# Optimization experiments

Measured on AMD Instinct MI355X. Metric: run time of the kernel, lower is better.

## Reference

```python
import jax, jax.numpy as jnp
import numpy as np

N, E, CIN, HOPS, HID, COUT = 50000, 800000, 64, 3, 256, 64

def setup_inputs() -> dict:
    key = jax.random.key(0)
    ks = jax.random.split(key, 8)
    x = jax.random.normal(ks[0], (N, CIN), dtype=jnp.float32)
    edge_index = jax.random.randint(ks[1], (2, E), 0, N, dtype=jnp.int64)
    def lin(k, fan_in, fan_out):
        bound = 1.0 / np.sqrt(fan_in)
        return jax.random.uniform(k, (fan_in, fan_out), jnp.float32, -bound, bound)
    W0 = lin(ks[2], CIN * (HOPS + 1), HID)
    W1 = lin(ks[3], HID, HID)
    W2 = lin(ks[4], HID, COUT)
    b0 = jnp.zeros((HID,), jnp.float32)
    b1 = jnp.zeros((HID,), jnp.float32)
    b2 = jnp.zeros((COUT,), jnp.float32)
    return {"x": x, "edge_index": edge_index, "W0": W0, "b0": b0, "W1": W1, "b1": b1, "W2": W2, "b2": b2}

def reference(x, edge_index, W0, b0, W1, b1, W2, b2):
    row, col = edge_index[0], edge_index[1]
    n = x.shape[0]
    # degree of destination nodes (degree(col, N))
    d = jax.ops.segment_sum(jnp.ones_like(col, dtype=jnp.float32), col, num_segments=n)
    d_norm_in = 1.0 / jnp.sqrt(d[col])   # per-edge
    d_norm_out = 1.0 / jnp.sqrt(d[row])
    value = d_norm_in * d_norm_out
    value = jnp.where(jnp.isfinite(value), value, 0.0)  # nan_to_num
    def spmm(h):
        # adj has entries at (col[e], row[e]) -> out[i] = sum_{e: col[e]=i} value[e] * h[row[e]]
        return jax.ops.segment_sum(value[:, None] * h[row], col, num_segments=n)
    emb = [x]
    h = x
    for _ in range(HOPS):
        h = spmm(h)
        emb.append(h)
    z = jnp.concatenate(emb, axis=1)  # [N, CIN*(HOPS+1)]
    # eval mode: dropout is identity, use_bn=False
    z = jax.nn.relu(z @ W0 + b0)
    z = jax.nn.relu(z @ W1 + b1)
    return z @ W2 + b2
```

## Files before the change

kernel.cpp:

```cpp
#include <hip/hip_runtime.h>


#define ZW 256
#define NCH 64

typedef __attribute__((ext_vector_type(8))) __bf16 bf16x8;
typedef __attribute__((ext_vector_type(4))) float f32x4;
typedef __attribute__((ext_vector_type(4))) unsigned short us4;

__device__ __forceinline__ unsigned f2bf(float f) {
    unsigned x = __float_as_uint(f);
    return (x + 0x7fffu + ((x >> 16) & 1u)) >> 16;
}
__device__ __forceinline__ unsigned pack_split(float v) {
    unsigned hb = f2bf(v);
    float hf = __uint_as_float(hb << 16);
    unsigned lb = f2bf(v - hf);
    return (hb << 16) | lb;
}
__device__ __forceinline__ float unpack_f(unsigned u) {
    return __uint_as_float(u & 0xffff0000u) + __uint_as_float(u << 16);
}


__global__ void init_kernel(const float* __restrict__ x, unsigned* __restrict__ zp,
                            int* __restrict__ deg, int N) {
    int stride = gridDim.x * blockDim.x;
    int total4 = N * 16;
    for (int idx = blockIdx.x * blockDim.x + threadIdx.x; idx < total4; idx += stride) {
        int n = idx >> 4, c4 = idx & 15;
        float4 v = *reinterpret_cast<const float4*>(x + (size_t)n * NCH + c4 * 4);
        uint4 o;
        o.x = pack_split(v.x); o.y = pack_split(v.y);
        o.z = pack_split(v.z); o.w = pack_split(v.w);
        *reinterpret_cast<uint4*>(zp + (size_t)n * ZW + c4 * 4) = o;
    }
    for (int idx = blockIdx.x * blockDim.x + threadIdx.x; idx < N; idx += stride)
        deg[idx] = 0;
}

__global__ void degree_kernel(const int* __restrict__ col, int* __restrict__ deg, int E) {
    int stride = gridDim.x * blockDim.x;
    for (int e = blockIdx.x * blockDim.x + threadIdx.x; e < E; e += stride)
        atomicAdd(&deg[col[e]], 1);
}

__global__ __launch_bounds__(1024) void scan_part_kernel(const int* __restrict__ deg,
                                                         int* __restrict__ off,
                                                         int* __restrict__ bsum, int N) {
    __shared__ int smem[1024];
    int tid = threadIdx.x;
    int i = blockIdx.x * 1024 + tid;
    int v = (i < N) ? deg[i] : 0;
    smem[tid] = v;
    __syncthreads();
    for (int o = 1; o < 1024; o <<= 1) {
        int t = (tid >= o) ? smem[tid - o] : 0;
        __syncthreads();
        smem[tid] += t;
        __syncthreads();
    }
    if (i < N) off[i] = smem[tid] - v;
    if (tid == 1023) bsum[blockIdx.x] = smem[1023];
}

__global__ void scan_tops_kernel(const int* __restrict__ bsum, int* __restrict__ btot, int nb) {
    int lane = threadIdx.x;
    int v = (lane < nb) ? bsum[lane] : 0;
    int incl = v;
    for (int o = 1; o < 64; o <<= 1) {
        int t = __shfl_up(incl, o);
        if (lane >= o) incl += t;
    }
    if (lane < nb) btot[lane] = incl - v;
    if (lane == 63) btot[nb] = incl;
}

__global__ __launch_bounds__(1024) void scan_add_kernel(int* __restrict__ off,
                                                        int* __restrict__ cur,
                                                        const int* __restrict__ btot,
                                                        int N, int nb) {
    int i = blockIdx.x * 1024 + threadIdx.x;
    if (i < N) {
        int o = off[i] + btot[blockIdx.x];
        off[i] = o;
        cur[i] = o;
    }
    if (i == 0) off[N] = btot[nb];
}

__global__ void scatter_kernel(const int* __restrict__ row, const int* __restrict__ col,
                               const int* __restrict__ deg, int* __restrict__ cursor,
                               int2* __restrict__ meta, int E) {
    int stride = gridDim.x * blockDim.x;
    for (int e = blockIdx.x * blockDim.x + threadIdx.x; e < E; e += stride) {
        int r = row[e];
        int c = col[e];
        int dc = deg[c];
        int dr = deg[r];
        float v = 0.0f;
        if (dc > 0 && dr > 0) v = rsqrtf((float)(dc * dr));
        int pos = atomicAdd(&cursor[c], 1);
        meta[pos] = make_int2(r, __float_as_int(v));
    }
}

__global__ void spmm_csr_kernel(const int* __restrict__ offsets, const int2* __restrict__ meta,
                                const unsigned* __restrict__ zin, unsigned* __restrict__ zout,
                                int N) {
    int lane = threadIdx.x & 63;
    int wave = (blockIdx.x * blockDim.x + threadIdx.x) >> 6;
    if (wave >= N) return;
    int start = offsets[wave];
    int end   = offsets[wave + 1];
    float acc = 0.0f;
    int j = start;
    for (; j + 2 <= end; j += 2) {
        int2 m0 = meta[j];
        int2 m1 = meta[j + 1];
        float h0 = unpack_f(zin[(size_t)m0.x * ZW + lane]);
        float h1 = unpack_f(zin[(size_t)m1.x * ZW + lane]);
        acc = fmaf(__int_as_float(m0.y), h0, acc);
        acc = fmaf(__int_as_float(m1.y), h1, acc);
    }
    if (j < end) {
        int2 m0 = meta[j];
        acc = fmaf(__int_as_float(m0.y), unpack_f(zin[(size_t)m0.x * ZW + lane]), acc);
    }
    zout[(size_t)wave * ZW + lane] = pack_split(acc);
}

__global__ void prep_w_kernel(const float* __restrict__ W0, const float* __restrict__ W1,
                              const float* __restrict__ W2, unsigned short* __restrict__ ws) {
    int idx = blockIdx.x * blockDim.x + threadIdx.x;
    if (idx >= 65536) return;
    int n = idx >> 8, k = idx & 255;
    unsigned p0 = pack_split(W0[(size_t)k * 256 + n]);
    ws[idx]          = (unsigned short)(p0 >> 16);
    ws[65536 + idx]  = (unsigned short)(p0 & 0xffff);
    unsigned p1 = pack_split(W1[(size_t)k * 256 + n]);
    ws[131072 + idx] = (unsigned short)(p1 >> 16);
    ws[196608 + idx] = (unsigned short)(p1 & 0xffff);
    if (idx < 16384) {
        int n2 = idx >> 8, k2 = idx & 255;
        unsigned p2 = pack_split(W2[(size_t)k2 * 64 + n2]);
        ws[262144 + idx] = (unsigned short)(p2 >> 16);
        ws[278528 + idx] = (unsigned short)(p2 & 0xffff);
    }
}

__global__ __launch_bounds__(256) void gemm256_kernel(
        const unsigned* __restrict__ Ap, const unsigned short* __restrict__ Wh,
        const unsigned short* __restrict__ Wl, const float* __restrict__ bias,
        unsigned* __restrict__ Cp, int M) {
    __shared__ unsigned short Ah[128][40];
    __shared__ unsigned short Al[128][40];
    __shared__ unsigned short Bh[128][40];
    __shared__ unsigned short Bl[128][40];

    int tid = threadIdx.x;
    int lane = tid & 63;
    int wid = tid >> 6;
    int wr = wid >> 1, wc = wid & 1;
    int bm = blockIdx.x * 128;
    int bn = blockIdx.y * 128;
    int l15 = lane & 15, kg = lane >> 4;

    f32x4 acc[4][4] = {};

    for (int k0 = 0; k0 < 256; k0 += 32) {
#pragma unroll
        for (int it = 0; it < 4; ++it) {
            int idx = it * 256 + tid;
            int row = idx >> 3, ch = idx & 7;
            int grow = bm + row; if (grow > M - 1) grow = M - 1;
            uint4 q = *reinterpret_cast<const uint4*>(Ap + (size_t)grow * 256 + k0 + ch * 4);
            us4 hi, lo;
            hi.x = (unsigned short)(q.x >> 16); lo.x = (unsigned short)q.x;
            hi.y = (unsigned short)(q.y >> 16); lo.y = (unsigned short)q.y;
            hi.z = (unsigned short)(q.z >> 16); lo.z = (unsigned short)q.z;
            hi.w = (unsigned short)(q.w >> 16); lo.w = (unsigned short)q.w;
            *reinterpret_cast<us4*>(&Ah[row][ch * 4]) = hi;
            *reinterpret_cast<us4*>(&Al[row][ch * 4]) = lo;
        }
#pragma unroll
        for (int it = 0; it < 2; ++it) {
            int idx = it * 256 + tid;
            int n = idx >> 2, ch = idx & 3;
            *reinterpret_cast<uint4*>(&Bh[n][ch * 8]) =
                *reinterpret_cast<const uint4*>(Wh + (size_t)(bn + n) * 256 + k0 + ch * 8);
            *reinterpret_cast<uint4*>(&Bl[n][ch * 8]) =
                *reinterpret_cast<const uint4*>(Wl + (size_t)(bn + n) * 256 + k0 + ch * 8);
        }
        __syncthreads();

        bf16x8 ah[4], al[4], bh[4], bl[4];
#pragma unroll
        for (int m = 0; m < 4; ++m) {
            int r = wr * 64 + m * 16 + l15;
            ah[m] = *reinterpret_cast<const bf16x8*>(&Ah[r][kg * 8]);
            al[m] = *reinterpret_cast<const bf16x8*>(&Al[r][kg * 8]);
        }
#pragma unroll
        for (int n = 0; n < 4; ++n) {
            int c = wc * 64 + n * 16 + l15;
            bh[n] = *reinterpret_cast<const bf16x8*>(&Bh[c][kg * 8]);
            bl[n] = *reinterpret_cast<const bf16x8*>(&Bl[c][kg * 8]);
        }
#pragma unroll
        for (int m = 0; m < 4; ++m)
#pragma unroll
            for (int n = 0; n < 4; ++n) {
                acc[m][n] = __builtin_amdgcn_mfma_f32_16x16x32_bf16(ah[m], bh[n], acc[m][n], 0, 0, 0);
                acc[m][n] = __builtin_amdgcn_mfma_f32_16x16x32_bf16(ah[m], bl[n], acc[m][n], 0, 0, 0);
                acc[m][n] = __builtin_amdgcn_mfma_f32_16x16x32_bf16(al[m], bh[n], acc[m][n], 0, 0, 0);
            }
        __syncthreads();
    }

#pragma unroll
    for (int n = 0; n < 4; ++n) {
        int col = bn + wc * 64 + n * 16 + l15;
        float bv = bias[col];
#pragma unroll
        for (int m = 0; m < 4; ++m) {
#pragma unroll
            for (int r = 0; r < 4; ++r) {
                int row = bm + wr * 64 + m * 16 + kg * 4 + r;
                if (row < M) {
                    float v = fmaxf(acc[m][n][r] + bv, 0.0f);
                    Cp[(size_t)row * 256 + col] = pack_split(v);
                }
            }
        }
    }
}

__global__ __launch_bounds__(256) void gemm64_kernel(
        const unsigned* __restrict__ Ap, const unsigned short* __restrict__ Wh,
        const unsigned short* __restrict__ Wl, const float* __restrict__ bias,
        float* __restrict__ out, int M) {
    __shared__ unsigned short Ah[128][40];
    __shared__ unsigned short Al[128][40];
    __shared__ unsigned short Bh[64][40];
    __shared__ unsigned short Bl[64][40];

    int tid = threadIdx.x;
    int lane = tid & 63;
    int wid = tid >> 6;
    int bm = blockIdx.x * 128;
    int l15 = lane & 15, kg = lane >> 4;

    f32x4 acc[2][4] = {};

    for (int k0 = 0; k0 < 256; k0 += 32) {
#pragma unroll
        for (int it = 0; it < 4; ++it) {
            int idx = it * 256 + tid;
            int row = idx >> 3, ch = idx & 7;
            int grow = bm + row; if (grow > M - 1) grow = M - 1;
            uint4 q = *reinterpret_cast<const uint4*>(Ap + (size_t)grow * 256 + k0 + ch * 4);
            us4 hi, lo;
            hi.x = (unsigned short)(q.x >> 16); lo.x = (unsigned short)q.x;
            hi.y = (unsigned short)(q.y >> 16); lo.y = (unsigned short)q.y;
            hi.z = (unsigned short)(q.z >> 16); lo.z = (unsigned short)q.z;
            hi.w = (unsigned short)(q.w >> 16); lo.w = (unsigned short)q.w;
            *reinterpret_cast<us4*>(&Ah[row][ch * 4]) = hi;
            *reinterpret_cast<us4*>(&Al[row][ch * 4]) = lo;
        }
        {
            int n = tid >> 2, ch = tid & 3;
            *reinterpret_cast<uint4*>(&Bh[n][ch * 8]) =
                *reinterpret_cast<const uint4*>(Wh + (size_t)n * 256 + k0 + ch * 8);
            *reinterpret_cast<uint4*>(&Bl[n][ch * 8]) =
                *reinterpret_cast<const uint4*>(Wl + (size_t)n * 256 + k0 + ch * 8);
        }
        __syncthreads();

        bf16x8 ah[2], al[2], bh[4], bl[4];
#pragma unroll
        for (int m = 0; m < 2; ++m) {
            int r = wid * 32 + m * 16 + l15;
            ah[m] = *reinterpret_cast<const bf16x8*>(&Ah[r][kg * 8]);
            al[m] = *reinterpret_cast<const bf16x8*>(&Al[r][kg * 8]);
        }
#pragma unroll
        for (int n = 0; n < 4; ++n) {
            int c = n * 16 + l15;
            bh[n] = *reinterpret_cast<const bf16x8*>(&Bh[c][kg * 8]);
            bl[n] = *reinterpret_cast<const bf16x8*>(&Bl[c][kg * 8]);
        }
#pragma unroll
        for (int m = 0; m < 2; ++m)
#pragma unroll
            for (int n = 0; n < 4; ++n) {
                acc[m][n] = __builtin_amdgcn_mfma_f32_16x16x32_bf16(ah[m], bh[n], acc[m][n], 0, 0, 0);
                acc[m][n] = __builtin_amdgcn_mfma_f32_16x16x32_bf16(ah[m], bl[n], acc[m][n], 0, 0, 0);
                acc[m][n] = __builtin_amdgcn_mfma_f32_16x16x32_bf16(al[m], bh[n], acc[m][n], 0, 0, 0);
            }
        __syncthreads();
    }

#pragma unroll
    for (int n = 0; n < 4; ++n) {
        int col = n * 16 + l15;
        float bv = bias[col];
#pragma unroll
        for (int m = 0; m < 2; ++m) {
#pragma unroll
            for (int r = 0; r < 4; ++r) {
                int row = bm + wid * 32 + m * 16 + kg * 4 + r;
                if (row < M) out[(size_t)row * 64 + col] = acc[m][n][r] + bv;
            }
        }
    }
}

extern "C" void kernel_launch(void* const* d_in, const int* in_sizes, int n_in,
                              void* d_out, int out_size, void* d_ws, size_t ws_size,
                              hipStream_t stream) {
    const float* x  = (const float*)d_in[0];
    const int* ei   = (const int*)d_in[1];
    const float* W0 = (const float*)d_in[2];
    const float* b0 = (const float*)d_in[3];
    const float* W1 = (const float*)d_in[4];
    const float* b1 = (const float*)d_in[5];
    const float* W2 = (const float*)d_in[6];
    const float* b2 = (const float*)d_in[7];
    float* out = (float*)d_out;

    const int N = in_sizes[0] / NCH;
    const int E = in_sizes[1] / 2;
    const int* row = ei;
    const int* col = ei + E;

    unsigned* zp = (unsigned*)d_ws;
    unsigned* hp = zp + (size_t)N * ZW;
    int* deg  = (int*)(hp + (size_t)N * ZW);
    int* off  = deg + N;
    int* cur  = off + N + 1;
    int* bsum = cur + N;
    int* btot = bsum + 64;
    unsigned short* wsp = (unsigned short*)(btot + 80);
    int2* meta = (int2*)hp;

    const int TB = 256;
    const int NB = (N + 1023) / 1024;

    prep_w_kernel<<<256, TB, 0, stream>>>(W0, W1, W2, wsp);
    init_kernel<<<2048, TB, 0, stream>>>(x, zp, deg, N);
    degree_kernel<<<1024, TB, 0, stream>>>(col, deg, E);
    scan_part_kernel<<<NB, 1024, 0, stream>>>(deg, off, bsum, N);
    scan_tops_kernel<<<1, 64, 0, stream>>>(bsum, btot, NB);
    scan_add_kernel<<<NB, 1024, 0, stream>>>(off, cur, btot, N, NB);
    scatter_kernel<<<1024, TB, 0, stream>>>(row, col, deg, cur, meta, E);

    int spmm_blocks = (N * 64 + TB - 1) / TB;
    for (int hop = 1; hop <= 3; ++hop) {
        const unsigned* zin = zp + (hop - 1) * NCH;
        unsigned* zout      = zp + hop * NCH;
        spmm_csr_kernel<<<spmm_blocks, TB, 0, stream>>>(off, meta, zin, zout, N);
    }

    int gblocks = (N + 127) / 128;
    dim3 g256(gblocks, 2);
    gemm256_kernel<<<g256, TB, 0, stream>>>(zp, wsp,          wsp + 65536,  b0, hp, N);
    gemm256_kernel<<<g256, TB, 0, stream>>>(hp, wsp + 131072, wsp + 196608, b1, zp, N);
    gemm64_kernel<<<gblocks, TB, 0, stream>>>(zp, wsp + 262144, wsp + 278528, b2, out, N);
}
```

Before: 430.4 us.

## Double-buffer GEMM tiles via direct global-to-LDS loads with XOR swizzle

Both MLP GEMM kernels now stage A and B tiles straight from global memory into LDS with global_load_lds, using two buffers so the next k-slice loads while the current one is computed. The A tile is kept packed in LDS and split into hi/lo bf16 parts at fragment-read time, with an XOR swizzle in place of padding to avoid bank conflicts. Occupancy hints are added to launch_bounds, the SpMM loop gains a 4-way unrolled gather, and the weight workspace is moved to sit before the degree arrays. The unpack work moves into the MFMA inner loop, which adds ALU and register pressure, and the swizzle and global_load_lds addressing must match exactly to stay correct.

```diff
diff --git a/kernel.cpp b/kernel.cpp
--- a/kernel.cpp
+++ b/kernel.cpp
@@ -6,7 +6,6 @@
 
 typedef __attribute__((ext_vector_type(8))) __bf16 bf16x8;
 typedef __attribute__((ext_vector_type(4))) float f32x4;
-typedef __attribute__((ext_vector_type(4))) unsigned short us4;
 
 __device__ __forceinline__ unsigned f2bf(float f) {
     unsigned x = __float_as_uint(f);
@@ -20,6 +19,12 @@
 }
 __device__ __forceinline__ float unpack_f(unsigned u) {
     return __uint_as_float(u & 0xffff0000u) + __uint_as_float(u << 16);
+}
+
+__device__ __forceinline__ void gload16(const void* g, void* l) {
+    __builtin_amdgcn_global_load_lds(
+        (const __attribute__((address_space(1))) unsigned*)g,
+        (__attribute__((address_space(3))) unsigned*)l, 16, 0, 0);
 }
 
 
@@ -115,6 +120,20 @@
     int end   = offsets[wave + 1];
     float acc = 0.0f;
     int j = start;
+    for (; j + 4 <= end; j += 4) {
+        int2 m0 = meta[j];
+        int2 m1 = meta[j + 1];
+        int2 m2 = meta[j + 2];
+        int2 m3 = meta[j + 3];
+        float h0 = unpack_f(zin[(size_t)m0.x * ZW + lane]);
+        float h1 = unpack_f(zin[(size_t)m1.x * ZW + lane]);
+        float h2 = unpack_f(zin[(size_t)m2.x * ZW + lane]);
+        float h3 = unpack_f(zin[(size_t)m3.x * ZW + lane]);
+        acc = fmaf(__int_as_float(m0.y), h0, acc);
+        acc = fmaf(__int_as_float(m1.y), h1, acc);
+        acc = fmaf(__int_as_float(m2.y), h2, acc);
+        acc = fmaf(__int_as_float(m3.y), h3, acc);
+    }
     for (; j + 2 <= end; j += 2) {
         int2 m0 = meta[j];
         int2 m1 = meta[j + 1];
@@ -149,14 +168,13 @@
     }
 }
 
-__global__ __launch_bounds__(256) void gemm256_kernel(
+__global__ __launch_bounds__(256, 2) void gemm256_kernel(
         const unsigned* __restrict__ Ap, const unsigned short* __restrict__ Wh,
         const unsigned short* __restrict__ Wl, const float* __restrict__ bias,
         unsigned* __restrict__ Cp, int M) {
-    __shared__ unsigned short Ah[128][40];
-    __shared__ unsigned short Al[128][40];
-    __shared__ unsigned short Bh[128][40];
-    __shared__ unsigned short Bl[128][40];
+    __shared__ unsigned Apl[2 * 128 * 32];
+    __shared__ unsigned short Bhl[2 * 128 * 32];
+    __shared__ unsigned short Bll[2 * 128 * 32];
 
     int tid = threadIdx.x;
     int lane = tid & 63;
@@ -168,67 +186,86 @@
 
     f32x4 acc[4][4] = {};
 
-    for (int k0 = 0; k0 < 256; k0 += 32) {
-#pragma unroll
-        for (int it = 0; it < 4; ++it) {
-            int idx = it * 256 + tid;
-            int row = idx >> 3, ch = idx & 7;
-            int grow = bm + row; if (grow > M - 1) grow = M - 1;
-            uint4 q = *reinterpret_cast<const uint4*>(Ap + (size_t)grow * 256 + k0 + ch * 4);
-            us4 hi, lo;
-            hi.x = (unsigned short)(q.x >> 16); lo.x = (unsigned short)q.x;
-            hi.y = (unsigned short)(q.y >> 16); lo.y = (unsigned short)q.y;
-            hi.z = (unsigned short)(q.z >> 16); lo.z = (unsigned short)q.z;
-            hi.w = (unsigned short)(q.w >> 16); lo.w = (unsigned short)q.w;
-            *reinterpret_cast<us4*>(&Ah[row][ch * 4]) = hi;
-            *reinterpret_cast<us4*>(&Al[row][ch * 4]) = lo;
-        }
-#pragma unroll
-        for (int it = 0; it < 2; ++it) {
-            int idx = it * 256 + tid;
-            int n = idx >> 2, ch = idx & 3;
-            *reinterpret_cast<uint4*>(&Bh[n][ch * 8]) =
-                *reinterpret_cast<const uint4*>(Wh + (size_t)(bn + n) * 256 + k0 + ch * 8);
-            *reinterpret_cast<uint4*>(&Bl[n][ch * 8]) =
-                *reinterpret_cast<const uint4*>(Wl + (size_t)(bn + n) * 256 + k0 + ch * 8);
-        }
-        __syncthreads();
-
-        bf16x8 ah[4], al[4], bh[4], bl[4];
+    auto STAGE = [&](int buf, int k0) {
+        unsigned* Ab = Apl + buf * (128 * 32);
+        unsigned short* Bhb = Bhl + buf * (128 * 32);
+        unsigned short* Blb = Bll + buf * (128 * 32);
+#pragma unroll
+        for (int i = 0; i < 4; ++i) {
+            int s = (wid * 4 + i) * 64 + lane;
+            int r = s >> 3, cp = s & 7;
+            int cl = cp ^ (r & 7);
+            int grow = bm + r; if (grow >= M) grow = M - 1;
+            gload16(Ap + (size_t)grow * 256 + k0 + cl * 4, Ab + (wid * 4 + i) * 256);
+        }
+#pragma unroll
+        for (int i = 0; i < 2; ++i) {
+            int s = (wid * 2 + i) * 64 + lane;
+            int n = s >> 2, cp = s & 3;
+            int cl = cp ^ ((n >> 1) & 3);
+            size_t goff = (size_t)(bn + n) * 256 + k0 + cl * 8;
+            gload16(Wh + goff, Bhb + (wid * 2 + i) * 512);
+            gload16(Wl + goff, Blb + (wid * 2 + i) * 512);
+        }
+    };
+
+    auto COMPUTE = [&](int buf) {
+        const unsigned* Ab = Apl + buf * (128 * 32);
+        const unsigned short* Bhb = Bhl + buf * (128 * 32);
+        const unsigned short* Blb = Bll + buf * (128 * 32);
+        bf16x8 bh[4], bl[4];
+#pragma unroll
+        for (int n4 = 0; n4 < 4; ++n4) {
+            int nn = wc * 64 + n4 * 16 + l15;
+            int c = kg ^ ((nn >> 1) & 3);
+            bh[n4] = *reinterpret_cast<const bf16x8*>(&Bhb[nn * 32 + c * 8]);
+            bl[n4] = *reinterpret_cast<const bf16x8*>(&Blb[nn * 32 + c * 8]);
+        }
 #pragma unroll
         for (int m = 0; m < 4; ++m) {
             int r = wr * 64 + m * 16 + l15;
-            ah[m] = *reinterpret_cast<const bf16x8*>(&Ah[r][kg * 8]);
-            al[m] = *reinterpret_cast<const bf16x8*>(&Al[r][kg * 8]);
-        }
-#pragma unroll
-        for (int n = 0; n < 4; ++n) {
-            int c = wc * 64 + n * 16 + l15;
-            bh[n] = *reinterpret_cast<const bf16x8*>(&Bh[c][kg * 8]);
-            bl[n] = *reinterpret_cast<const bf16x8*>(&Bl[c][kg * 8]);
-        }
-#pragma unroll
-        for (int m = 0; m < 4; ++m)
-#pragma unroll
-            for (int n = 0; n < 4; ++n) {
-                acc[m][n] = __builtin_amdgcn_mfma_f32_16x16x32_bf16(ah[m], bh[n], acc[m][n], 0, 0, 0);
-                acc[m][n] = __builtin_amdgcn_mfma_f32_16x16x32_bf16(ah[m], bl[n], acc[m][n], 0, 0, 0);
-                acc[m][n] = __builtin_amdgcn_mfma_f32_16x16x32_bf16(al[m], bh[n], acc[m][n], 0, 0, 0);
+            int c0 = (2 * kg) ^ (r & 7);
+            int c1 = (2 * kg + 1) ^ (r & 7);
+            uint4 q0 = *reinterpret_cast<const uint4*>(&Ab[r * 32 + c0 * 4]);
+            uint4 q1 = *reinterpret_cast<const uint4*>(&Ab[r * 32 + c1 * 4]);
+            union { bf16x8 v; unsigned short s[8]; } ah, al;
+            ah.s[0] = (unsigned short)(q0.x >> 16); al.s[0] = (unsigned short)q0.x;
+            ah.s[1] = (unsigned short)(q0.y >> 16); al.s[1] = (unsigned short)q0.y;
+            ah.s[2] = (unsigned short)(q0.z >> 16); al.s[2] = (unsigned short)q0.z;
+            ah.s[3] = (unsigned short)(q0.w >> 16); al.s[3] = (unsigned short)q0.w;
+            ah.s[4] = (unsigned short)(q1.x >> 16); al.s[4] = (unsigned short)q1.x;
+            ah.s[5] = (unsigned short)(q1.y >> 16); al.s[5] = (unsigned short)q1.y;
+            ah.s[6] = (unsigned short)(q1.z >> 16); al.s[6] = (unsigned short)q1.z;
+            ah.s[7] = (unsigned short)(q1.w >> 16); al.s[7] = (unsigned short)q1.w;
+#pragma unroll
+            for (int n4 = 0; n4 < 4; ++n4) {
+                acc[m][n4] = __builtin_amdgcn_mfma_f32_16x16x32_bf16(ah.v, bh[n4], acc[m][n4], 0, 0, 0);
+                acc[m][n4] = __builtin_amdgcn_mfma_f32_16x16x32_bf16(ah.v, bl[n4], acc[m][n4], 0, 0, 0);
+                acc[m][n4] = __builtin_amdgcn_mfma_f32_16x16x32_bf16(al.v, bh[n4], acc[m][n4], 0, 0, 0);
             }
+        }
+    };
+
+    STAGE(0, 0);
+    __syncthreads();
+#pragma unroll
+    for (int t = 0; t < 8; ++t) {
+        if (t < 7) STAGE((t + 1) & 1, (t + 1) * 32);
+        COMPUTE(t & 1);
         __syncthreads();
     }
 
 #pragma unroll
-    for (int n = 0; n < 4; ++n) {
-        int col = bn + wc * 64 + n * 16 + l15;
+    for (int n4 = 0; n4 < 4; ++n4) {
+        int col = bn + wc * 64 + n4 * 16 + l15;
         float bv = bias[col];
 #pragma unroll
         for (int m = 0; m < 4; ++m) {
 #pragma unroll
-            for (int r = 0; r < 4; ++r) {
-                int row = bm + wr * 64 + m * 16 + kg * 4 + r;
+            for (int rr = 0; rr < 4; ++rr) {
+                int row = bm + wr * 64 + m * 16 + kg * 4 + rr;
                 if (row < M) {
-                    float v = fmaxf(acc[m][n][r] + bv, 0.0f);
+                    float v = fmaxf(acc[m][n4][rr] + bv, 0.0f);
                     Cp[(size_t)row * 256 + col] = pack_split(v);
                 }
             }
@@ -236,14 +273,13 @@
     }
 }
 
-__global__ __launch_bounds__(256) void gemm64_kernel(
+__global__ __launch_bounds__(256, 3) void gemm64_kernel(
         const unsigned* __restrict__ Ap, const unsigned short* __restrict__ Wh,
         const unsigned short* __restrict__ Wl, const float* __restrict__ bias,
         float* __restrict__ out, int M) {
-    __shared__ unsigned short Ah[128][40];
-    __shared__ unsigned short Al[128][40];
-    __shared__ unsigned short Bh[64][40];
-    __shared__ unsigned short Bl[64][40];
+    __shared__ unsigned Apl[2 * 128 * 32];
+    __shared__ unsigned short Bhl[2 * 64 * 32];
+    __shared__ unsigned short Bll[2 * 64 * 32];
 
     int tid = threadIdx.x;
     int lane = tid & 63;
@@ -253,64 +289,84 @@
 
     f32x4 acc[2][4] = {};
 
-    for (int k0 = 0; k0 < 256; k0 += 32) {
-#pragma unroll
-        for (int it = 0; it < 4; ++it) {
-            int idx = it * 256 + tid;
-            int row = idx >> 3, ch = idx & 7;
-            int grow = bm + row; if (grow > M - 1) grow = M - 1;
-            uint4 q = *reinterpret_cast<const uint4*>(Ap + (size_t)grow * 256 + k0 + ch * 4);
-            us4 hi, lo;
-            hi.x = (unsigned short)(q.x >> 16); lo.x = (unsigned short)q.x;
-            hi.y = (unsigned short)(q.y >> 16); lo.y = (unsigned short)q.y;
-            hi.z = (unsigned short)(q.z >> 16); lo.z = (unsigned short)q.z;
-            hi.w = (unsigned short)(q.w >> 16); lo.w = (unsigned short)q.w;
-            *reinterpret_cast<us4*>(&Ah[row][ch * 4]) = hi;
-            *reinterpret_cast<us4*>(&Al[row][ch * 4]) = lo;
+    auto STAGE = [&](int buf, int k0) {
+        unsigned* Ab = Apl + buf * (128 * 32);
+        unsigned short* Bhb = Bhl + buf * (64 * 32);
+        unsigned short* Blb = Bll + buf * (64 * 32);
+#pragma unroll
+        for (int i = 0; i < 4; ++i) {
+            int s = (wid * 4 + i) * 64 + lane;
+            int r = s >> 3, cp = s & 7;
+            int cl = cp ^ (r & 7);
+            int grow = bm + r; if (grow >= M) grow = M - 1;
+            gload16(Ap + (size_t)grow * 256 + k0 + cl * 4, Ab + (wid * 4 + i) * 256);
         }
         {
-            int n = tid >> 2, ch = tid & 3;
-            *reinterpret_cast<uint4*>(&Bh[n][ch * 8]) =
-                *reinterpret_cast<const uint4*>(Wh + (size_t)n * 256 + k0 + ch * 8);
-            *reinterpret_cast<uint4*>(&Bl[n][ch * 8]) =
-                *reinterpret_cast<const uint4*>(Wl + (size_t)n * 256 + k0 + ch * 8);
-        }
-        __syncthreads();
-
-        bf16x8 ah[2], al[2], bh[4], bl[4];
+            int s = wid * 64 + lane;
+            int n = s >> 2, cp = s & 3;
+            int cl = cp ^ ((n >> 1) & 3);
+            size_t goff = (size_t)n * 256 + k0 + cl * 8;
+            gload16(Wh + goff, Bhb + wid * 512);
+            gload16(Wl + goff, Blb + wid * 512);
+        }
+    };
+
+    auto COMPUTE = [&](int buf) {
+        const unsigned* Ab = Apl + buf * (128 * 32);
+        const unsigned short* Bhb = Bhl + buf * (64 * 32);
+        const unsigned short* Blb = Bll + buf * (64 * 32);
+        bf16x8 bh[4], bl[4];
+#pragma unroll
+        for (int n4 = 0; n4 < 4; ++n4) {
+            int nn = n4 * 16 + l15;
+            int c = kg ^ ((nn >> 1) & 3);
+            bh[n4] = *reinterpret_cast<const bf16x8*>(&Bhb[nn * 32 + c * 8]);
+            bl[n4] = *reinterpret_cast<const bf16x8*>(&Blb[nn * 32 + c * 8]);
+        }
 #pragma unroll
         for (int m = 0; m < 2; ++m) {
             int r = wid * 32 + m * 16 + l15;
-            ah[m] = *reinterpret_cast<const bf16x8*>(&Ah[r][kg * 8]);
-            al[m] = *reinterpret_cast<const bf16x8*>(&Al[r][kg * 8]);
-        }
-#pragma unroll
-        for (int n = 0; n < 4; ++n) {
-            int c = n * 16 + l15;
-            bh[n] = *reinterpret_cast<const bf16x8*>(&Bh[c][kg * 8]);
-            bl[n] = *reinterpret_cast<const bf16x8*>(&Bl[c][kg * 8]);
-        }
-#pragma unroll
-        for (int m = 0; m < 2; ++m)
-#pragma unroll
-            for (int n = 0; n < 4; ++n) {
-                acc[m][n] = __builtin_amdgcn_mfma_f32_16x16x32_bf16(ah[m], bh[n], acc[m][n], 0, 0, 0);
-                acc[m][n] = __builtin_amdgcn_mfma_f32_16x16x32_bf16(ah[m], bl[n], acc[m][n], 0, 0, 0);
-                acc[m][n] = __builtin_amdgcn_mfma_f32_16x16x32_bf16(al[m], bh[n], acc[m][n], 0, 0, 0);
+            int c0 = (2 * kg) ^ (r & 7);
+            int c1 = (2 * kg + 1) ^ (r & 7);
+            uint4 q0 = *reinterpret_cast<const uint4*>(&Ab[r * 32 + c0 * 4]);
+            uint4 q1 = *reinterpret_cast<const uint4*>(&Ab[r * 32 + c1 * 4]);
+            union { bf16x8 v; unsigned short s[8]; } ah, al;
+            ah.s[0] = (unsigned short)(q0.x >> 16); al.s[0] = (unsigned short)q0.x;
+            ah.s[1] = (unsigned short)(q0.y >> 16); al.s[1] = (unsigned short)q0.y;
+            ah.s[2] = (unsigned short)(q0.z >> 16); al.s[2] = (unsigned short)q0.z;
+            ah.s[3] = (unsigned short)(q0.w >> 16); al.s[3] = (unsigned short)q0.w;
+            ah.s[4] = (unsigned short)(q1.x >> 16); al.s[4] = (unsigned short)q1.x;
+            ah.s[5] = (unsigned short)(q1.y >> 16); al.s[5] = (unsigned short)q1.y;
+            ah.s[6] = (unsigned short)(q1.z >> 16); al.s[6] = (unsigned short)q1.z;
+            ah.s[7] = (unsigned short)(q1.w >> 16); al.s[7] = (unsigned short)q1.w;
+#pragma unroll
+            for (int n4 = 0; n4 < 4; ++n4) {
+                acc[m][n4] = __builtin_amdgcn_mfma_f32_16x16x32_bf16(ah.v, bh[n4], acc[m][n4], 0, 0, 0);
+                acc[m][n4] = __builtin_amdgcn_mfma_f32_16x16x32_bf16(ah.v, bl[n4], acc[m][n4], 0, 0, 0);
+                acc[m][n4] = __builtin_amdgcn_mfma_f32_16x16x32_bf16(al.v, bh[n4], acc[m][n4], 0, 0, 0);
             }
+        }
+    };
+
+    STAGE(0, 0);
+    __syncthreads();
+#pragma unroll
+    for (int t = 0; t < 8; ++t) {
+        if (t < 7) STAGE((t + 1) & 1, (t + 1) * 32);
+        COMPUTE(t & 1);
         __syncthreads();
     }
 
 #pragma unroll
-    for (int n = 0; n < 4; ++n) {
-        int col = n * 16 + l15;
+    for (int n4 = 0; n4 < 4; ++n4) {
+        int col = n4 * 16 + l15;
         float bv = bias[col];
 #pragma unroll
         for (int m = 0; m < 2; ++m) {
 #pragma unroll
-            for (int r = 0; r < 4; ++r) {
-                int row = bm + wid * 32 + m * 16 + kg * 4 + r;
-                if (row < M) out[(size_t)row * 64 + col] = acc[m][n][r] + bv;
+            for (int rr = 0; rr < 4; ++rr) {
+                int row = bm + wid * 32 + m * 16 + kg * 4 + rr;
+                if (row < M) out[(size_t)row * 64 + col] = acc[m][n4][rr] + bv;
             }
         }
     }
@@ -336,12 +392,12 @@
 
     unsigned* zp = (unsigned*)d_ws;
     unsigned* hp = zp + (size_t)N * ZW;
-    int* deg  = (int*)(hp + (size_t)N * ZW);
+    unsigned short* wsp = (unsigned short*)(hp + (size_t)N * ZW);
+    int* deg  = (int*)(wsp + 294912);
     int* off  = deg + N;
     int* cur  = off + N + 1;
     int* bsum = cur + N;
     int* btot = bsum + 64;
-    unsigned short* wsp = (unsigned short*)(btot + 80);
     int2* meta = (int2*)hp;
 
     const int TB = 256;
```

After: 386.0 us. 10.3% less time.
